# Kernel tuning notes

Measured on AMD Instinct MI355X. Metric: run time of the kernel, lower is better.

## Reference

```python
import jax, jax.numpy as jnp
import numpy as np

D_MODEL, N_HEADS, D_C, D_COMP, D_ROPE = 2048, 16, 512, 768, 64
D_HEAD = D_MODEL // N_HEADS  # 128
B, S = 2, 2048
ROPE_THETA = 10000.0


def _rope_cos_sin(seq_len, dim):
    # frequencies for pairwise complex rotation, dim = per-head rope dim (even)
    inv_freq = 1.0 / (ROPE_THETA ** (jnp.arange(0, dim, 2, dtype=jnp.float32) / dim))
    t = jnp.arange(seq_len, dtype=jnp.float32)
    ang = t[:, None] * inv_freq[None, :]  # [S, dim/2]
    return jnp.cos(ang), jnp.sin(ang)


def _apply_rope(x, cos, sin):
    # x: [B, S, H, dr]; rotate consecutive pairs (view_as_complex semantics)
    x1, x2 = x[..., 0::2], x[..., 1::2]
    c = cos[None, :, None, :]
    s = sin[None, :, None, :]
    y1 = x1 * c - x2 * s
    y2 = x1 * s + x2 * c
    return jnp.stack([y1, y2], axis=-1).reshape(x.shape)


def setup_inputs() -> dict:
    key = jax.random.key(0)
    ks = jax.random.split(key, 9)
    sc = 0.02
    return {
        "x": jax.random.normal(ks[0], (B, S, D_MODEL), jnp.float32),
        "Wd": jax.random.normal(ks[1], (D_MODEL, D_C), jnp.float32) * sc,
        "bd": jnp.zeros((D_C,), jnp.float32),
        "Wu": jax.random.normal(ks[2], (D_C, N_HEADS * D_HEAD), jnp.float32) * sc,
        "bu": jnp.zeros((N_HEADS * D_HEAD,), jnp.float32),
        "Wqd": jax.random.normal(ks[3], (D_MODEL, D_COMP), jnp.float32) * sc,
        "bqd": jnp.zeros((D_COMP,), jnp.float32),
        "Wqu": jax.random.normal(ks[4], (D_COMP, N_HEADS * D_HEAD), jnp.float32) * sc,
        "bqu": jnp.zeros((N_HEADS * D_HEAD,), jnp.float32),
        "Wqr": jax.random.normal(ks[5], (D_COMP, N_HEADS * D_ROPE), jnp.float32) * sc,
        "bqr": jnp.zeros((N_HEADS * D_ROPE,), jnp.float32),
        "Wkr": jax.random.normal(ks[6], (D_MODEL, N_HEADS * D_ROPE), jnp.float32) * sc,
        "bkr": jnp.zeros((N_HEADS * D_ROPE,), jnp.float32),
        "Wo": jax.random.normal(ks[7], (N_HEADS * D_HEAD, D_MODEL), jnp.float32) * sc,
        "bo": jnp.zeros((D_MODEL,), jnp.float32),
    }


def reference(x, Wd, bd, Wu, bu, Wqd, bqd, Wqu, bqu, Wqr, bqr, Wkr, bkr, Wo, bo):
    b, s, _ = x.shape
    # low-rank KV compression
    kv_c = x @ Wd + bd                                   # [B,S,d_c]
    kv_up = (kv_c @ Wu + bu).reshape(b, s, N_HEADS, D_HEAD)  # shared K-content / V
    # low-rank Q compression
    q_cmp = x @ Wqd + bqd                                # [B,S,d_comp]
    q_c = (q_cmp @ Wqu + bqu).reshape(b, s, N_HEADS, D_HEAD)
    # decoupled RoPE branches
    cos, sin = _rope_cos_sin(s, D_ROPE)
    q_r = _apply_rope((q_cmp @ Wqr + bqr).reshape(b, s, N_HEADS, D_ROPE), cos, sin)
    k_r = _apply_rope((x @ Wkr + bkr).reshape(b, s, N_HEADS, D_ROPE), cos, sin)
    q = jnp.concatenate([q_c, q_r], axis=-1)             # [B,S,H,dh+dr]
    k = jnp.concatenate([kv_up, k_r], axis=-1)           # [B,S,H,dh+dr]
    scale = 1.0 / np.sqrt(D_HEAD).astype(np.float32)
    scores = jnp.einsum('bqhd,bkhd->bhqk', q, k) * scale  # [B,H,S,S]
    probs = jax.nn.softmax(scores, axis=-1)
    out = jnp.einsum('bhqk,bkhd->bqhd', probs, kv_up)    # v == kv_up (as in source)
    out = out.reshape(b, s, N_HEADS * D_HEAD)
    return out @ Wo + bo
```

## Files before the change

### kernel.cpp

```cpp
#include <hip/hip_runtime.h>
#include <cmath>

typedef __bf16 bf16;
typedef __bf16 bf16x8 __attribute__((ext_vector_type(8)));
typedef __bf16 bf16x4 __attribute__((ext_vector_type(4)));
typedef __bf16 bf16x2 __attribute__((ext_vector_type(2)));
typedef float f32x4 __attribute__((ext_vector_type(4)));
typedef float f32x16 __attribute__((ext_vector_type(16)));
typedef int i32x4 __attribute__((ext_vector_type(4)));
typedef int i32x2 __attribute__((ext_vector_type(2)));

#define S_LEN 2048
#define QK_LD 3072

__device__ __forceinline__ void async_copy16(const bf16* g, bf16* l) {
    __builtin_amdgcn_global_load_lds(
        (const __attribute__((address_space(1))) void*)g,
        (__attribute__((address_space(3))) void*)l, 16, 0, 0);
}

__device__ __forceinline__ unsigned packbf(float a, float b) {
    bf16x2 v; v[0] = (bf16)a; v[1] = (bf16)b;
    return __builtin_bit_cast(unsigned, v);
}

__global__ __launch_bounds__(256) void cast_f32_bf16(const float* __restrict__ in,
                                                     bf16* __restrict__ out) {
    size_t i = ((size_t)blockIdx.x * 256 + threadIdx.x) * 8;
    float4 a = *(const float4*)(in + i);
    float4 b = *(const float4*)(in + i + 4);
    bf16x8 v;
    v[0] = (bf16)a.x; v[1] = (bf16)a.y; v[2] = (bf16)a.z; v[3] = (bf16)a.w;
    v[4] = (bf16)b.x; v[5] = (bf16)b.y; v[6] = (bf16)b.z; v[7] = (bf16)b.w;
    *(bf16x8*)(out + i) = v;
}

struct TSeg { const float* src; bf16* dst; int K, N, blk0; };
struct TArgs { TSeg s[7]; };

__global__ __launch_bounds__(256) void transpose_all(TArgs a) {
    __shared__ float tile[64][68];
    int b = blockIdx.x, si = 0;
#pragma unroll
    for (int i = 1; i < 7; ++i) if (b >= a.s[i].blk0) si = i;
    TSeg sg = a.s[si];
    int local = b - sg.blk0;
    int kTiles = sg.K >> 6;
    int kt = local % kTiles, nt = local / kTiles;
    int k0 = kt * 64, n0 = nt * 64;
    int K = sg.K, N = sg.N;
    int t = threadIdx.x;
#pragma unroll
    for (int i = 0; i < 4; ++i) {
        int c = t + i * 256;
        int r = c >> 4, off = (c & 15) * 4;
        float4 v = *(const float4*)(sg.src + (size_t)(k0 + r) * N + n0 + off);
        tile[r][off] = v.x; tile[r][off + 1] = v.y;
        tile[r][off + 2] = v.z; tile[r][off + 3] = v.w;
    }
    __syncthreads();
#pragma unroll
    for (int i = 0; i < 2; ++i) {
        int c = t + i * 256;
        int nr = c >> 3, koff = (c & 7) * 8;
        bf16x8 v;
#pragma unroll
        for (int j = 0; j < 8; ++j) v[j] = (bf16)tile[koff + j][nr];
        *(bf16x8*)(sg.dst + (size_t)(n0 + nr) * K + k0 + koff) = v;
    }
}

__global__ __launch_bounds__(256) void setup_small(const float* __restrict__ bd,
                                                   const float* __restrict__ bqd,
                                                   const float* __restrict__ bkr,
                                                   const float* __restrict__ bqu,
                                                   const float* __restrict__ bqr,
                                                   float* __restrict__ bcat,
                                                   float2* __restrict__ tab) {
    if (blockIdx.x < 21) {
        int i = blockIdx.x * 256 + threadIdx.x;
        if (i < 512) bcat[i] = bd[i];
        else if (i < 1280) bcat[i] = bqd[i - 512];
        else if (i < 2304) bcat[i] = bkr[i - 1280];
        else if (i < 4352) bcat[i] = bqu[i - 2304];
        else if (i < 5376) bcat[i] = bqr[i - 4352];
    } else {
        int id = (blockIdx.x - 21) * 256 + threadIdx.x;
        int s = id >> 5, i = id & 31;
        float f = expf(-0.2878231366242557f * (float)i);
        float ang = (float)s * f;
        tab[id] = make_float2(cosf(ang), sinf(ang));
    }
}

__device__ __forceinline__ void gemm_core(const bf16* __restrict__ A, int lda,
                                          const bf16* __restrict__ Bt,
                                          const float* __restrict__ bias,
                                          void* __restrict__ out0,
                                          void* __restrict__ out1,
                                          int Ndim, int Kdim, int mode,
                                          const float2* __restrict__ tab,
                                          int bn, int bm, bf16* As, bf16* Bs) {
    int t = threadIdx.x;
    int w = t >> 6, lane = t & 63;
    int wm = (w >> 1) * 64, wn = (w & 1) * 64;
    int l15 = lane & 15, q4 = lane >> 4;
    f32x4 acc[4][4] = {};

    int lrow = lane >> 2;
    int lcol = (lane & 3) * 8;
    int c0 = w * 2, c1 = w * 2 + 1;
    const bf16* aS0 = A  + (size_t)(bm * 128 + c0 * 16 + lrow) * lda + lcol;
    const bf16* aS1 = A  + (size_t)(bm * 128 + c1 * 16 + lrow) * lda + lcol;
    const bf16* bS0 = Bt + (size_t)(bn * 128 + c0 * 16 + lrow) * Kdim + lcol;
    const bf16* bS1 = Bt + (size_t)(bn * 128 + c1 * 16 + lrow) * Kdim + lcol;
    bf16* aD0 = &As[c0 * 512]; bf16* aD1 = &As[c1 * 512];
    bf16* bD0 = &Bs[c0 * 512]; bf16* bD1 = &Bs[c1 * 512];

    for (int kt = 0; kt < Kdim; kt += 32) {
        async_copy16(aS0 + kt, aD0);
        async_copy16(aS1 + kt, aD1);
        async_copy16(bS0 + kt, bD0);
        async_copy16(bS1 + kt, bD1);
        __syncthreads();
        bf16x8 af[4], bfr[4];
#pragma unroll
        for (int mb = 0; mb < 4; ++mb)
            af[mb] = *(const bf16x8*)&As[(wm + mb * 16 + l15) * 32 + q4 * 8];
#pragma unroll
        for (int nb = 0; nb < 4; ++nb)
            bfr[nb] = *(const bf16x8*)&Bs[(wn + nb * 16 + l15) * 32 + q4 * 8];
#pragma unroll
        for (int mb = 0; mb < 4; ++mb)
#pragma unroll
            for (int nb = 0; nb < 4; ++nb)
                acc[mb][nb] = __builtin_amdgcn_mfma_f32_16x16x32_bf16(
                    af[mb], bfr[nb], acc[mb][nb], 0, 0, 0);
        __syncthreads();
    }

#pragma unroll
    for (int mb = 0; mb < 4; ++mb) {
        int row = bm * 128 + wm + mb * 16 + q4 * 4;
#pragma unroll
        for (int nb = 0; nb < 4; ++nb) {
            int col = bn * 128 + wn + nb * 16 + l15;
            float bv = bias[col];
            if (mode == 1) {
#pragma unroll
                for (int r = 0; r < 4; ++r)
                    ((float*)out0)[(size_t)(row + r) * Ndim + col] = acc[mb][nb][r] + bv;
            } else if (mode == 4) {
                if (col < 1280) {
#pragma unroll
                    for (int r = 0; r < 4; ++r)
                        ((bf16*)out0)[(size_t)(row + r) * 2304 + col] =
                            (bf16)(acc[mb][nb][r] + bv);
                } else {
                    int rel = col - 1280;
                    int hh = rel >> 6, idx = rel & 63, ii = idx >> 1, odd = idx & 1;
#pragma unroll
                    for (int r = 0; r < 4; ++r) {
                        float vv = acc[mb][nb][r] + bv;
                        float pp = __shfl_xor(vv, 1, 64);
                        float2 cs = tab[((row + r) & 2047) * 32 + ii];
                        float o = vv * cs.x + (odd ? pp * cs.y : -pp * cs.y);
                        ((bf16*)out1)[(size_t)(row + r) * QK_LD + hh * 192 + 128 + idx] =
                            (bf16)o;
                    }
                }
            } else if (mode == 5) {
                if (col < 2048) {
                    int hh = col >> 7, dd = col & 127;
#pragma unroll
                    for (int r = 0; r < 4; ++r)
                        ((bf16*)out0)[(size_t)(row + r) * QK_LD + hh * 192 + dd] =
                            (bf16)(acc[mb][nb][r] + bv);
                } else {
                    int rel = col - 2048;
                    int hh = rel >> 6, idx = rel & 63, ii = idx >> 1, odd = idx & 1;
#pragma unroll
                    for (int r = 0; r < 4; ++r) {
                        float vv = acc[mb][nb][r] + bv;
                        float pp = __shfl_xor(vv, 1, 64);
                        float2 cs = tab[((row + r) & 2047) * 32 + ii];
                        float o = vv * cs.x + (odd ? pp * cs.y : -pp * cs.y);
                        ((bf16*)out0)[(size_t)(row + r) * QK_LD + hh * 192 + 128 + idx] =
                            (bf16)o;
                    }
                }
            } else {
                int hh = col >> 7, dd = col & 127;
                bf16x4 pack;
#pragma unroll
                for (int r = 0; r < 4; ++r) {
                    float vv = acc[mb][nb][r] + bv;
                    ((bf16*)out0)[(size_t)(row + r) * QK_LD + hh * 192 + dd] = (bf16)vv;
                    pack[r] = (bf16)vv;
                }
                int bidx = row >> 11, srow = row & 2047;
                *(bf16x4*)((bf16*)out1 +
                           ((size_t)(bidx * 16 + hh) * 128 + dd) * S_LEN + srow) = pack;
            }
        }
    }
}

__device__ __forceinline__ void xcd_chunk(int gx, int& bn, int& bm) {
    int lin = blockIdx.y * gx + blockIdx.x;
    int nwg = gx * gridDim.y;
    int chunk = nwg >> 3;
    int nl = (lin & 7) * chunk + (lin >> 3);
    bn = nl % gx;
    bm = nl / gx;
}

__global__ __launch_bounds__(256) void gemm_bt(const bf16* __restrict__ A, int lda,
                                               const bf16* __restrict__ Bt,
                                               const float* __restrict__ bias,
                                               void* __restrict__ out0,
                                               void* __restrict__ out1,
                                               int Ndim, int Kdim, int mode,
                                               const float2* __restrict__ tab) {
    __shared__ bf16 As[128 * 32];
    __shared__ bf16 Bs[128 * 32];
    int bn, bm;
    xcd_chunk(gridDim.x, bn, bm);
    gemm_core(A, lda, Bt, bias, out0, out1, Ndim, Kdim, mode, tab,
              bn, bm, As, Bs);
}

__global__ __launch_bounds__(256) void gemm_up(const bf16* __restrict__ xproj,
                                               const bf16* __restrict__ WuT,
                                               const float* __restrict__ bu,
                                               void* __restrict__ kbuf,
                                               void* __restrict__ vt,
                                               const bf16* __restrict__ W2T,
                                               const float* __restrict__ bq,
                                               void* __restrict__ qbuf,
                                               const float2* __restrict__ tab) {
    __shared__ bf16 As[128 * 32];
    __shared__ bf16 Bs[128 * 32];
    int bn, bm;
    xcd_chunk(gridDim.x, bn, bm);
    if (bn < 16)
        gemm_core(xproj, 2304, WuT, bu, kbuf, vt, 2048, 512, 6, tab,
                  bn, bm, As, Bs);
    else
        gemm_core(xproj + 512, 2304, W2T, bq, qbuf, nullptr, 3072, 768, 5, tab,
                  bn - 16, bm, As, Bs);
}

__global__ __launch_bounds__(256, 2) void attn(const bf16* __restrict__ qbuf,
                                               const bf16* __restrict__ kbuf,
                                               const bf16* __restrict__ vt,
                                               bf16* __restrict__ attnout) {
    __shared__ bf16 Ks[2][32 * 192];
    __shared__ bf16 Vs[2][128 * 32];
    int bh = blockIdx.x;
    int qt = blockIdx.y;
    int b = bh >> 4, h = bh & 15;
    int t = threadIdx.x, w = t >> 6, lane = t & 63;
    int l31 = lane & 31, hl = lane >> 5;
    const float scale2 = 0.1275174333f;

    bf16x8 qf[12];
    {
        size_t rbase = (size_t)(b * S_LEN + qt * 128 + w * 32 + l31) * QK_LD
                       + h * 192 + hl * 8;
#pragma unroll
        for (int c = 0; c < 12; ++c)
            qf[c] = *(const bf16x8*)(qbuf + rbase + c * 16);
    }

    f32x16 oacc[4] = {};
    float denom = 0.f;
    const bf16* kb_base = kbuf + (size_t)b * S_LEN * QK_LD + h * 192;
    const bf16* vt_base = vt + (size_t)bh * 128 * S_LEN;

    int kg_[3], klA_[3], klB_[3], vg_[2], vlA_[2], vlB_[2];
#pragma unroll
    for (int i = 0; i < 3; ++i) {
        int c = t + (i << 8);
        int kr = c / 24, u = c % 24;
        kg_[i] = kr * QK_LD + u * 8;
        int m = kr & 15;
        klA_[i] = kr * 192 + (((2 * u) ^ m) << 2);
        klB_[i] = kr * 192 + (((2 * u + 1) ^ m) << 2);
    }
#pragma unroll
    for (int i = 0; i < 2; ++i) {
        int c = t + (i << 8);
        int vd = c >> 2, u = c & 3;
        vg_[i] = vd * S_LEN + u * 8;
        int line = vd >> 1, lm = line & 15;
        int sl = 8 * (vd & 1) + 2 * u;
        vlA_[i] = line * 64 + ((sl ^ lm) << 2);
        vlB_[i] = line * 64 + (((sl + 1) ^ lm) << 2);
    }

    int mK = l31 & 15;
    int kRow = l31 * 192;
    int vLM = l31 >> 1;
    int vSlotB = 8 * (l31 & 1) + 2 * hl;

    i32x4 kreg[3], vreg[2];
#pragma unroll
    for (int i = 0; i < 3; ++i) kreg[i] = *(const i32x4*)(kb_base + kg_[i]);
#pragma unroll
    for (int i = 0; i < 2; ++i) vreg[i] = *(const i32x4*)(vt_base + vg_[i]);
#pragma unroll
    for (int i = 0; i < 3; ++i) {
        i32x2 lo; lo[0] = kreg[i][0]; lo[1] = kreg[i][1];
        i32x2 hi; hi[0] = kreg[i][2]; hi[1] = kreg[i][3];
        *(i32x2*)&Ks[0][klA_[i]] = lo;
        *(i32x2*)&Ks[0][klB_[i]] = hi;
    }
#pragma unroll
    for (int i = 0; i < 2; ++i) {
        i32x2 lo; lo[0] = vreg[i][0]; lo[1] = vreg[i][1];
        i32x2 hi; hi[0] = vreg[i][2]; hi[1] = vreg[i][3];
        *(i32x2*)&Vs[0][vlA_[i]] = lo;
        *(i32x2*)&Vs[0][vlB_[i]] = hi;
    }
    __syncthreads();

    int cur = 0;
    for (int kt = 0; kt < 64; ++kt) {
        if (kt < 63) {
            const bf16* kb = kb_base + (size_t)(kt + 1) * 32 * QK_LD;
#pragma unroll
            for (int i = 0; i < 3; ++i) kreg[i] = *(const i32x4*)(kb + kg_[i]);
#pragma unroll
            for (int i = 0; i < 2; ++i)
                vreg[i] = *(const i32x4*)(vt_base + (kt + 1) * 32 + vg_[i]);
        }

        f32x16 sacc = {};
        __builtin_amdgcn_s_setprio(1);
#pragma unroll
        for (int c = 0; c < 12; ++c) {
            int u0 = 4 * c + 2 * hl;
            i32x2 lo = *(const i32x2*)&Ks[cur][kRow + ((u0 ^ mK) << 2)];
            i32x2 hi = *(const i32x2*)&Ks[cur][kRow + (((u0 + 1) ^ mK) << 2)];
            i32x4 kv; kv[0] = lo[0]; kv[1] = lo[1]; kv[2] = hi[0]; kv[3] = hi[1];
            bf16x8 kb = __builtin_bit_cast(bf16x8, kv);
            sacc = __builtin_amdgcn_mfma_f32_32x32x16_bf16(kb, qf[c], sacc, 0, 0, 0);
        }
        __builtin_amdgcn_s_setprio(0);

        unsigned W[8], pw[8];
#pragma unroll
        for (int m = 0; m < 8; ++m) {
            float e0 = __builtin_amdgcn_exp2f(fminf(sacc[2 * m] * scale2, 72.0f));
            float e1 = __builtin_amdgcn_exp2f(fminf(sacc[2 * m + 1] * scale2, 72.0f));
            denom += e0 + e1;
            W[m] = packbf(e0, e1);
        }
#pragma unroll
        for (int m = 0; m < 8; ++m)
            pw[m] = (unsigned)__shfl_xor((int)W[m], 32, 64);
        bf16x8 paf[2];
#pragma unroll
        for (int s = 0; s < 2; ++s) {
            unsigned A = hl ? pw[4 * s + 2] : W[4 * s + 0];
            unsigned B = hl ? pw[4 * s + 3] : W[4 * s + 1];
            unsigned C = hl ? W[4 * s + 2] : pw[4 * s + 0];
            unsigned D = hl ? W[4 * s + 3] : pw[4 * s + 1];
            i32x4 di; di[0] = (int)A; di[1] = (int)B; di[2] = (int)C; di[3] = (int)D;
            paf[s] = __builtin_bit_cast(bf16x8, di);
        }

        __builtin_amdgcn_s_setprio(1);
#pragma unroll
        for (int dg = 0; dg < 4; ++dg) {
#pragma unroll
            for (int s = 0; s < 2; ++s) {
                int line = dg * 16 + (l31 >> 1);
                int s0 = (vSlotB + 4 * s) ^ vLM;
                int s1 = (vSlotB + 4 * s + 1) ^ vLM;
                i32x2 lo = *(const i32x2*)&Vs[cur][line * 64 + (s0 << 2)];
                i32x2 hi = *(const i32x2*)&Vs[cur][line * 64 + (s1 << 2)];
                i32x4 vv; vv[0] = lo[0]; vv[1] = lo[1]; vv[2] = hi[0]; vv[3] = hi[1];
                bf16x8 vb = __builtin_bit_cast(bf16x8, vv);
                oacc[dg] = __builtin_amdgcn_mfma_f32_32x32x16_bf16(
                    paf[s], vb, oacc[dg], 0, 0, 0);
            }
        }
        __builtin_amdgcn_s_setprio(0);

        if (kt < 63) {
#pragma unroll
            for (int i = 0; i < 3; ++i) {
                i32x2 lo; lo[0] = kreg[i][0]; lo[1] = kreg[i][1];
                i32x2 hi; hi[0] = kreg[i][2]; hi[1] = kreg[i][3];
                *(i32x2*)&Ks[cur ^ 1][klA_[i]] = lo;
                *(i32x2*)&Ks[cur ^ 1][klB_[i]] = hi;
            }
#pragma unroll
            for (int i = 0; i < 2; ++i) {
                i32x2 lo; lo[0] = vreg[i][0]; lo[1] = vreg[i][1];
                i32x2 hi; hi[0] = vreg[i][2]; hi[1] = vreg[i][3];
                *(i32x2*)&Vs[cur ^ 1][vlA_[i]] = lo;
                *(i32x2*)&Vs[cur ^ 1][vlB_[i]] = hi;
            }
        }
        __syncthreads();
        cur ^= 1;
    }

    denom += __shfl_xor(denom, 32, 64);

#pragma unroll
    for (int r = 0; r < 16; ++r) {
        int rowl = (r & 3) + 8 * (r >> 2) + 4 * hl;
        float dv = __shfl(denom, rowl, 64);
        float inv = 1.0f / dv;
        int row = qt * 128 + w * 32 + rowl;
#pragma unroll
        for (int dg = 0; dg < 4; ++dg) {
            int col = h * 128 + dg * 32 + l31;
            attnout[(size_t)(b * S_LEN + row) * 2048 + col] =
                (bf16)(oacc[dg][r] * inv);
        }
    }
}

extern "C" void kernel_launch(void* const* d_in, const int* in_sizes, int n_in,
                              void* d_out, int out_size, void* d_ws, size_t ws_size,
                              hipStream_t stream) {
    const float* x   = (const float*)d_in[0];
    const float* Wd  = (const float*)d_in[1];
    const float* bd  = (const float*)d_in[2];
    const float* Wu  = (const float*)d_in[3];
    const float* bu  = (const float*)d_in[4];
    const float* Wqd = (const float*)d_in[5];
    const float* bqd = (const float*)d_in[6];
    const float* Wqu = (const float*)d_in[7];
    const float* bqu = (const float*)d_in[8];
    const float* Wqr = (const float*)d_in[9];
    const float* bqr = (const float*)d_in[10];
    const float* Wkr = (const float*)d_in[11];
    const float* bkr = (const float*)d_in[12];
    const float* Wo  = (const float*)d_in[13];
    const float* bo  = (const float*)d_in[14];
    float* out = (float*)d_out;

    char* p = (char*)d_ws;
    auto alloc = [&](size_t n) { char* r = p; p += (n + 255) & ~(size_t)255; return r; };
    bf16* xb    = (bf16*)alloc((size_t)4096 * 2048 * 2);
    bf16* W1T   = (bf16*)alloc((size_t)2304 * 2048 * 2);
    bf16* W2T   = (bf16*)alloc((size_t)3072 * 768 * 2);
    bf16* WuT   = (bf16*)alloc((size_t)2048 * 512 * 2);
    bf16* WoT   = (bf16*)alloc((size_t)2048 * 2048 * 2);
    bf16* xproj = (bf16*)alloc((size_t)4096 * 2304 * 2);
    bf16* qbuf  = (bf16*)alloc((size_t)4096 * 3072 * 2);
    bf16* kbuf  = (bf16*)alloc((size_t)4096 * 3072 * 2);
    bf16* vt    = (bf16*)alloc((size_t)32 * 128 * 2048 * 2);
    bf16* aout  = (bf16*)alloc((size_t)4096 * 2048 * 2);
    float* bcat = (float*)alloc((size_t)5376 * 4);
    float2* tab = (float2*)alloc((size_t)65536 * 8);

    cast_f32_bf16<<<dim3(4096), dim3(256), 0, stream>>>(x, xb);

    TArgs ta;
    ta.s[0] = {Wd,  W1T,                       2048, 512,  0};
    ta.s[1] = {Wqd, W1T + (size_t)512 * 2048,  2048, 768,  256};
    ta.s[2] = {Wkr, W1T + (size_t)1280 * 2048, 2048, 1024, 640};
    ta.s[3] = {Wqu, W2T,                       768,  2048, 1152};
    ta.s[4] = {Wqr, W2T + (size_t)2048 * 768,  768,  1024, 1536};
    ta.s[5] = {Wu,  WuT,                       512,  2048, 1728};
    ta.s[6] = {Wo,  WoT,                       2048, 2048, 1984};
    transpose_all<<<dim3(3008), dim3(256), 0, stream>>>(ta);
    setup_small<<<dim3(277), dim3(256), 0, stream>>>(bd, bqd, bkr, bqu, bqr, bcat, tab);

    gemm_bt<<<dim3(18, 32), dim3(256), 0, stream>>>(xb, 2048, W1T, bcat,
                                                    xproj, kbuf, 2304, 2048, 4, tab);
    gemm_up<<<dim3(40, 32), dim3(256), 0, stream>>>(xproj, WuT, bu, kbuf, vt,
                                                    W2T, bcat + 2304, qbuf, tab);

    attn<<<dim3(32, 16), dim3(256), 0, stream>>>(qbuf, kbuf, vt, aout);

    gemm_bt<<<dim3(16, 32), dim3(256), 0, stream>>>(aout, 2048, WoT, bo,
                                                    out, nullptr, 2048, 2048, 1, tab);
}
```

Measured before the change: 434.8 us.

## Split attention key range across two blocks with a separate reduction kernel

The attention kernel now processes half the keys per block, doubling the grid, and writes unnormalized fp32 partial outputs and denominators to workspace. A new reduce kernel sums the two halves, normalizes, and writes bf16 output. Launch bounds are raised to 4 blocks per CU to increase occupancy. This adds extra global traffic for the fp32 partials and a kernel launch, and risks register spills under the tighter bound.

```diff
diff --git a/kernel.cpp b/kernel.cpp
--- a/kernel.cpp
+++ b/kernel.cpp
@@ -251,14 +251,16 @@
                   bn - 16, bm, As, Bs);
 }
 
-__global__ __launch_bounds__(256, 2) void attn(const bf16* __restrict__ qbuf,
+__global__ __launch_bounds__(256, 4) void attn(const bf16* __restrict__ qbuf,
                                                const bf16* __restrict__ kbuf,
                                                const bf16* __restrict__ vt,
-                                               bf16* __restrict__ attnout) {
+                                               float* __restrict__ pacc,
+                                               float* __restrict__ dn) {
     __shared__ bf16 Ks[2][32 * 192];
     __shared__ bf16 Vs[2][128 * 32];
     int bh = blockIdx.x;
-    int qt = blockIdx.y;
+    int qt = blockIdx.y & 15;
+    int ck = blockIdx.y >> 4;
     int b = bh >> 4, h = bh & 15;
     int t = threadIdx.x, w = t >> 6, lane = t & 63;
     int l31 = lane & 31, hl = lane >> 5;
@@ -275,8 +277,9 @@
 
     f32x16 oacc[4] = {};
     float denom = 0.f;
-    const bf16* kb_base = kbuf + (size_t)b * S_LEN * QK_LD + h * 192;
-    const bf16* vt_base = vt + (size_t)bh * 128 * S_LEN;
+    const bf16* kb_base = kbuf + (size_t)b * S_LEN * QK_LD + h * 192
+                          + (size_t)ck * 1024 * QK_LD;
+    const bf16* vt_base = vt + (size_t)bh * 128 * S_LEN + ck * 1024;
 
     int kg_[3], klA_[3], klB_[3], vg_[2], vlA_[2], vlB_[2];
 #pragma unroll
@@ -326,8 +329,8 @@
     __syncthreads();
 
     int cur = 0;
-    for (int kt = 0; kt < 64; ++kt) {
-        if (kt < 63) {
+    for (int kt = 0; kt < 32; ++kt) {
+        if (kt < 31) {
             const bf16* kb = kb_base + (size_t)(kt + 1) * 32 * QK_LD;
 #pragma unroll
             for (int i = 0; i < 3; ++i) kreg[i] = *(const i32x4*)(kb + kg_[i]);
@@ -389,7 +392,7 @@
         }
         __builtin_amdgcn_s_setprio(0);
 
-        if (kt < 63) {
+        if (kt < 31) {
 #pragma unroll
             for (int i = 0; i < 3; ++i) {
                 i32x2 lo; lo[0] = kreg[i][0]; lo[1] = kreg[i][1];
@@ -411,18 +414,40 @@
 
     denom += __shfl_xor(denom, 32, 64);
 
+    int blk = (bh * 16 + qt) * 2 + ck;
+    float* pt = pacc + (size_t)blk * 16384;
+    if (hl == 0) dn[blk * 128 + w * 32 + l31] = denom;
 #pragma unroll
     for (int r = 0; r < 16; ++r) {
         int rowl = (r & 3) + 8 * (r >> 2) + 4 * hl;
-        float dv = __shfl(denom, rowl, 64);
-        float inv = 1.0f / dv;
-        int row = qt * 128 + w * 32 + rowl;
-#pragma unroll
-        for (int dg = 0; dg < 4; ++dg) {
-            int col = h * 128 + dg * 32 + l31;
-            attnout[(size_t)(b * S_LEN + row) * 2048 + col] =
-                (bf16)(oacc[dg][r] * inv);
-        }
+#pragma unroll
+        for (int dg = 0; dg < 4; ++dg)
+            pt[(w * 32 + rowl) * 128 + dg * 32 + l31] = oacc[dg][r];
+    }
+}
+
+__global__ __launch_bounds__(256) void attn_reduce(const float* __restrict__ pacc,
+                                                   const float* __restrict__ dn,
+                                                   bf16* __restrict__ aout) {
+    int tile = blockIdx.x;
+    int bh = tile >> 4, qt = tile & 15;
+    int b = bh >> 4, h = bh & 15;
+    const float* p0 = pacc + (size_t)tile * 2 * 16384;
+    const float* p1 = p0 + 16384;
+    const float* d0 = dn + tile * 2 * 128;
+    const float* d1 = d0 + 128;
+    int t = threadIdx.x;
+    int col = (t & 31) * 4, rbase = t >> 5;
+#pragma unroll
+    for (int it = 0; it < 16; ++it) {
+        int r = it * 8 + rbase;
+        float inv = 1.0f / (d0[r] + d1[r]);
+        f32x4 a = *(const f32x4*)(p0 + r * 128 + col);
+        f32x4 c = *(const f32x4*)(p1 + r * 128 + col);
+        bf16x4 o;
+#pragma unroll
+        for (int j = 0; j < 4; ++j) o[j] = (bf16)((a[j] + c[j]) * inv);
+        *(bf16x4*)(aout + (size_t)(b * S_LEN + qt * 128 + r) * 2048 + h * 128 + col) = o;
     }
 }
 
@@ -448,18 +473,22 @@
 
     char* p = (char*)d_ws;
     auto alloc = [&](size_t n) { char* r = p; p += (n + 255) & ~(size_t)255; return r; };
-    bf16* xb    = (bf16*)alloc((size_t)4096 * 2048 * 2);
-    bf16* W1T   = (bf16*)alloc((size_t)2304 * 2048 * 2);
-    bf16* W2T   = (bf16*)alloc((size_t)3072 * 768 * 2);
-    bf16* WuT   = (bf16*)alloc((size_t)2048 * 512 * 2);
     bf16* WoT   = (bf16*)alloc((size_t)2048 * 2048 * 2);
-    bf16* xproj = (bf16*)alloc((size_t)4096 * 2304 * 2);
     bf16* qbuf  = (bf16*)alloc((size_t)4096 * 3072 * 2);
     bf16* kbuf  = (bf16*)alloc((size_t)4096 * 3072 * 2);
     bf16* vt    = (bf16*)alloc((size_t)32 * 128 * 2048 * 2);
     bf16* aout  = (bf16*)alloc((size_t)4096 * 2048 * 2);
     float* bcat = (float*)alloc((size_t)5376 * 4);
     float2* tab = (float2*)alloc((size_t)65536 * 8);
+    float* dn   = (float*)alloc((size_t)131072 * 4);
+    char* mark = p;
+    bf16* xb    = (bf16*)alloc((size_t)4096 * 2048 * 2);
+    bf16* W1T   = (bf16*)alloc((size_t)2304 * 2048 * 2);
+    bf16* W2T   = (bf16*)alloc((size_t)3072 * 768 * 2);
+    bf16* WuT   = (bf16*)alloc((size_t)2048 * 512 * 2);
+    bf16* xproj = (bf16*)alloc((size_t)4096 * 2304 * 2);
+    float* pacc = (float*)mark;
+    p = mark + (size_t)1024 * 16384 * 4;
 
     cast_f32_bf16<<<dim3(4096), dim3(256), 0, stream>>>(x, xb);
 
@@ -479,7 +508,8 @@
     gemm_up<<<dim3(40, 32), dim3(256), 0, stream>>>(xproj, WuT, bu, kbuf, vt,
                                                     W2T, bcat + 2304, qbuf, tab);
 
-    attn<<<dim3(32, 16), dim3(256), 0, stream>>>(qbuf, kbuf, vt, aout);
+    attn<<<dim3(32, 32), dim3(256), 0, stream>>>(qbuf, kbuf, vt, pacc, dn);
+    attn_reduce<<<dim3(512), dim3(256), 0, stream>>>(pacc, dn, aout);
 
     gemm_bt<<<dim3(16, 32), dim3(256), 0, stream>>>(aout, 2048, WoT, bo,
                                                     out, nullptr, 2048, 2048, 1, tab);
```

Measured after the change: 829.9 us. 90.9% more time.
